# Kernel optimization log

Measured on AMD Instinct MI355X. Metric: run time of the kernel, lower is better.

The kernel has to match this reference:

```python
import jax, jax.numpy as jnp
import numpy as np

LN2 = 0.693147
TARGET_MEAN = 200.0
TARGET_STD = 40.0
BUFFER_SIZE = 1000
TARGET_LOG_MEAN = float(np.log2(TARGET_MEAN))
TARGET_LOG_STD = TARGET_STD / (TARGET_MEAN * LN2)
BLOCK = 33_554_432  # 2**25 pitch frames


def setup_inputs() -> dict:
    key = jax.random.key(0)
    k1, k2 = jax.random.split(key)
    u = jax.random.uniform(k1, (BLOCK,), dtype=jnp.float32)
    unvoiced = jax.random.uniform(k2, (BLOCK,), dtype=jnp.float32) < 0.2
    # realistic F0 range 80-480 Hz, zeros for unvoiced frames
    pitch = jnp.where(unvoiced, 0.0, 80.0 + 400.0 * u)
    return {"pitch_values": pitch}


def reference(pitch_values):
    # State is the freshly-initialized tracker: empty buffer, buffer_idx = 0.
    N = pitch_values.shape[0]
    B = BUFFER_SIZE
    valid = pitch_values > 0
    # log2 of valid pitches (safe for invalid lanes)
    log_p = jnp.log2(jnp.where(valid, pitch_values, 1.0))

    # rank of each valid element among valid elements (scatter order)
    rank = jnp.cumsum(valid.astype(jnp.int32)) - 1          # [N]
    n_valid = jnp.maximum(rank[-1] + 1, 0)
    # dense array of valid log-pitches ordered by rank (unique indices)
    dense_idx = jnp.where(valid, rank, N)                    # N is OOB -> dropped
    dense = jnp.zeros((N,), pitch_values.dtype).at[dense_idx].set(log_p, mode='drop')

    # circular buffer: slot j holds the LAST (max-rank) value written there
    slot = jnp.where(valid, rank % B, B)                     # B is OOB -> dropped
    winner = jnp.full((B,), -1, jnp.int32).at[slot].max(rank, mode='drop')
    filled = winner >= 0
    buf = jnp.where(filled, dense[jnp.clip(winner, 0, N - 1)], 0.0)

    count = jnp.minimum(n_valid, B)
    cnt_f = jnp.maximum(count, 1).astype(pitch_values.dtype)
    mean = jnp.sum(buf) / cnt_f
    mean = jnp.where(count > 0, mean, 0.0)                   # init mean = 0.0
    var = jnp.sum(jnp.where(filled, (buf - mean) ** 2, 0.0)) / jnp.maximum(count - 1, 1).astype(pitch_values.dtype)
    std = jnp.where(count > 1, jnp.sqrt(var), 1.0)           # unbiased std (torch default)
    std = jnp.maximum(std, 1e-7)

    normalized = (log_p - mean) / std
    scaled = normalized * TARGET_LOG_STD + TARGET_LOG_MEAN
    return jnp.where(valid, jnp.exp2(scaled), 0.0)
```

## Files before the change

### kernel.cpp

```cpp
#include <hip/hip_runtime.h>
#include <math.h>

#define BUF_SIZE 1000
#define TARGET_LOG_MEAN 7.6438561897747395f
#define TARGET_LOG_STD  (40.0f / (200.0f * 0.693147f))

__global__ __launch_bounds__(256) void fused_kernel(
    const float* __restrict__ pitch, float* __restrict__ out, long long n) {
    const int tid  = threadIdx.x;
    const int lane = tid & 63;
    const int wid  = tid >> 6;

    __shared__ int    s_wtot[4];
    __shared__ double s_red[8];
    __shared__ float  s_sb[2];

    double sum = 0.0, sumsq = 0.0;
    long long count_so_far = 0;

    const unsigned long long above =
        (lane == 63) ? 0ULL : (~0ULL << (lane + 1));

    const long long nchunks = (n + 1023) >> 10;
    for (long long c = nchunks - 1; c >= 0; --c) {
        const long long base = (c << 10) + (long long)tid * 4;
        float v[4];
        int valid[4];
#pragma unroll
        for (int j = 0; j < 4; ++j) {
            const long long idx = base + j;
            const float p = (idx < n) ? pitch[idx] : 0.0f;
            v[j] = p;
            valid[j] = (p > 0.0f) ? 1 : 0;
        }

        int suff_wave = 0;
        int wtot = 0;
#pragma unroll
        for (int j = 0; j < 4; ++j) {
            const unsigned long long m = __ballot(valid[j]);
            suff_wave += __popcll(m & above);
            wtot      += __popcll(m);
        }
        if (lane == 0) s_wtot[wid] = wtot;
        __syncthreads();
        int suff_after = suff_wave;
        int total = 0;
#pragma unroll
        for (int w = 0; w < 4; ++w) {
            const int t = s_wtot[w];
            total += t;
            if (w > wid) suff_after += t;
        }

        int r = 0;
#pragma unroll
        for (int j = 3; j >= 0; --j) {
            if (valid[j]) {
                const long long rev = count_so_far + suff_after + r;
                if (rev < BUF_SIZE) {
                    const double lp = (double)__log2f(v[j]);
                    sum   += lp;
                    sumsq += lp * lp;
                }
                r++;
            }
        }
        count_so_far += total;
        __syncthreads();
        if (count_so_far >= BUF_SIZE) break;
    }

#pragma unroll
    for (int off = 32; off > 0; off >>= 1) {
        sum   += __shfl_down(sum,   off, 64);
        sumsq += __shfl_down(sumsq, off, 64);
    }
    if (lane == 0) { s_red[wid] = sum; s_red[4 + wid] = sumsq; }
    __syncthreads();
    if (tid == 0) {
        const double tsum   = s_red[0] + s_red[1] + s_red[2] + s_red[3];
        const double tsumsq = s_red[4] + s_red[5] + s_red[6] + s_red[7];
        const long long count =
            (count_so_far < BUF_SIZE) ? count_so_far : BUF_SIZE;
        float mean, stdv;
        if (count == 0) {
            mean = 0.0f;
            stdv = 1.0f;
        } else {
            mean = (float)(tsum / (double)count);
            if (count > 1) {
                double var = (tsumsq - tsum * tsum / (double)count) /
                             (double)(count - 1);
                if (var < 0.0) var = 0.0;
                stdv = (float)sqrt(var);
            } else {
                stdv = 1.0f;
            }
        }
        if (stdv < 1e-7f) stdv = 1e-7f;
        const float scale = TARGET_LOG_STD / stdv;
        s_sb[0] = scale;
        s_sb[1] = TARGET_LOG_MEAN - mean * scale;
    }
    __syncthreads();
    const float scale = s_sb[0];
    const float bias  = s_sb[1];

    const float4* __restrict__ in4  = (const float4*)pitch;
    float4* __restrict__       out4 = (float4*)out;
    const long long n4     = n >> 2;
    const long long gid    = (long long)blockIdx.x * blockDim.x + tid;
    const long long stride = (long long)gridDim.x * blockDim.x;

    for (long long k = gid; k < n4; k += stride) {
        const float4 p = in4[k];
        float4 o;
        o.x = (p.x > 0.0f) ? exp2f(fmaf(__log2f(p.x), scale, bias)) : 0.0f;
        o.y = (p.y > 0.0f) ? exp2f(fmaf(__log2f(p.y), scale, bias)) : 0.0f;
        o.z = (p.z > 0.0f) ? exp2f(fmaf(__log2f(p.z), scale, bias)) : 0.0f;
        o.w = (p.w > 0.0f) ? exp2f(fmaf(__log2f(p.w), scale, bias)) : 0.0f;
        out4[k] = o;
    }

    const long long tail_start = n4 << 2;
    for (long long k = tail_start + gid; k < n; k += stride) {
        const float p = pitch[k];
        out[k] = (p > 0.0f) ? exp2f(fmaf(__log2f(p), scale, bias)) : 0.0f;
    }
}

extern "C" void kernel_launch(void* const* d_in, const int* in_sizes, int n_in,
                              void* d_out, int out_size, void* d_ws, size_t ws_size,
                              hipStream_t stream) {
    const float* pitch = (const float*)d_in[0];
    float* out = (float*)d_out;
    const long long n = (long long)in_sizes[0];

    int blocks = 2048;
    const long long n4 = n / 4;
    if ((long long)blocks * 256 > n4 + 255) {
        blocks = (int)((n4 + 255) / 256);
        if (blocks < 1) blocks = 1;
    }
    fused_kernel<<<blocks, 256, 0, stream>>>(pitch, out, n);
}
```

Baseline: 233.8 us.

## Prefetch first tile before stats scan and software-pipeline the elementwise pass

Each block now issues loads for its first 4 float4 vectors before the backward suffix scan that computes the buffer statistics, so that memory latency overlaps the scan. The main loop is restructured so each thread handles 4 float4 per iteration while prefetching the next iteration's data into registers (double buffering). The backward scan is widened to 8 elements per thread with vector loads, and launch bounds are tightened to 6 waves per SIMD. This raises register pressure in exchange for more memory-level parallelism.

```diff
diff --git a/kernel.cpp b/kernel.cpp
--- a/kernel.cpp
+++ b/kernel.cpp
@@ -5,7 +5,7 @@
 #define TARGET_LOG_MEAN 7.6438561897747395f
 #define TARGET_LOG_STD  (40.0f / (200.0f * 0.693147f))
 
-__global__ __launch_bounds__(256) void fused_kernel(
+__global__ __launch_bounds__(256, 6) void fused_kernel(
     const float* __restrict__ pitch, float* __restrict__ out, long long n) {
     const int tid  = threadIdx.x;
     const int lane = tid & 63;
@@ -15,29 +15,48 @@
     __shared__ double s_red[8];
     __shared__ float  s_sb[2];
 
+    const float4* __restrict__ in4  = (const float4*)pitch;
+    float4* __restrict__       out4 = (float4*)out;
+    const long long n4      = n >> 2;
+    const long long CHUNK4  = 1024;
+    const long long gstride = (long long)gridDim.x * CHUNK4;
+    const long long kbase   = (long long)blockIdx.x * CHUNK4 + tid;
+
+    float4 a0 = {0,0,0,0}, a1 = {0,0,0,0}, a2 = {0,0,0,0}, a3 = {0,0,0,0};
+    if (kbase < n4)       a0 = in4[kbase];
+    if (kbase + 256 < n4) a1 = in4[kbase + 256];
+    if (kbase + 512 < n4) a2 = in4[kbase + 512];
+    if (kbase + 768 < n4) a3 = in4[kbase + 768];
+
     double sum = 0.0, sumsq = 0.0;
     long long count_so_far = 0;
 
     const unsigned long long above =
         (lane == 63) ? 0ULL : (~0ULL << (lane + 1));
 
-    const long long nchunks = (n + 1023) >> 10;
+    const long long nchunks = (n + 2047) >> 11;
     for (long long c = nchunks - 1; c >= 0; --c) {
-        const long long base = (c << 10) + (long long)tid * 4;
-        float v[4];
-        int valid[4];
+        const long long base = (c << 11) + (long long)tid * 8;
+        float v[8];
+        if (base + 8 <= n) {
+            const float4 x = in4[(base >> 2)];
+            const float4 y = in4[(base >> 2) + 1];
+            v[0] = x.x; v[1] = x.y; v[2] = x.z; v[3] = x.w;
+            v[4] = y.x; v[5] = y.y; v[6] = y.z; v[7] = y.w;
+        } else {
 #pragma unroll
-        for (int j = 0; j < 4; ++j) {
-            const long long idx = base + j;
-            const float p = (idx < n) ? pitch[idx] : 0.0f;
-            v[j] = p;
-            valid[j] = (p > 0.0f) ? 1 : 0;
+            for (int j = 0; j < 8; ++j) {
+                const long long idx = base + j;
+                v[j] = (idx < n) ? pitch[idx] : 0.0f;
+            }
         }
 
+        int valid[8];
         int suff_wave = 0;
         int wtot = 0;
 #pragma unroll
-        for (int j = 0; j < 4; ++j) {
+        for (int j = 0; j < 8; ++j) {
+            valid[j] = (v[j] > 0.0f) ? 1 : 0;
             const unsigned long long m = __ballot(valid[j]);
             suff_wave += __popcll(m & above);
             wtot      += __popcll(m);
@@ -55,7 +74,7 @@
 
         int r = 0;
 #pragma unroll
-        for (int j = 3; j >= 0; --j) {
+        for (int j = 7; j >= 0; --j) {
             if (valid[j]) {
                 const long long rev = count_so_far + suff_after + r;
                 if (rev < BUF_SIZE) {
@@ -107,26 +126,48 @@
     const float scale = s_sb[0];
     const float bias  = s_sb[1];
 
-    const float4* __restrict__ in4  = (const float4*)pitch;
-    float4* __restrict__       out4 = (float4*)out;
-    const long long n4     = n >> 2;
-    const long long gid    = (long long)blockIdx.x * blockDim.x + tid;
-    const long long stride = (long long)gridDim.x * blockDim.x;
+    long long k = kbase;
+    while (k < n4) {
+        const long long kn = k + gstride;
+        float4 b0 = {0,0,0,0}, b1 = {0,0,0,0}, b2 = {0,0,0,0}, b3 = {0,0,0,0};
+        if (kn < n4)       b0 = in4[kn];
+        if (kn + 256 < n4) b1 = in4[kn + 256];
+        if (kn + 512 < n4) b2 = in4[kn + 512];
+        if (kn + 768 < n4) b3 = in4[kn + 768];
 
-    for (long long k = gid; k < n4; k += stride) {
-        const float4 p = in4[k];
-        float4 o;
-        o.x = (p.x > 0.0f) ? exp2f(fmaf(__log2f(p.x), scale, bias)) : 0.0f;
-        o.y = (p.y > 0.0f) ? exp2f(fmaf(__log2f(p.y), scale, bias)) : 0.0f;
-        o.z = (p.z > 0.0f) ? exp2f(fmaf(__log2f(p.z), scale, bias)) : 0.0f;
-        o.w = (p.w > 0.0f) ? exp2f(fmaf(__log2f(p.w), scale, bias)) : 0.0f;
-        out4[k] = o;
+        float4 o0, o1, o2, o3;
+        o0.x = (a0.x > 0.0f) ? exp2f(fmaf(__log2f(a0.x), scale, bias)) : 0.0f;
+        o0.y = (a0.y > 0.0f) ? exp2f(fmaf(__log2f(a0.y), scale, bias)) : 0.0f;
+        o0.z = (a0.z > 0.0f) ? exp2f(fmaf(__log2f(a0.z), scale, bias)) : 0.0f;
+        o0.w = (a0.w > 0.0f) ? exp2f(fmaf(__log2f(a0.w), scale, bias)) : 0.0f;
+        o1.x = (a1.x > 0.0f) ? exp2f(fmaf(__log2f(a1.x), scale, bias)) : 0.0f;
+        o1.y = (a1.y > 0.0f) ? exp2f(fmaf(__log2f(a1.y), scale, bias)) : 0.0f;
+        o1.z = (a1.z > 0.0f) ? exp2f(fmaf(__log2f(a1.z), scale, bias)) : 0.0f;
+        o1.w = (a1.w > 0.0f) ? exp2f(fmaf(__log2f(a1.w), scale, bias)) : 0.0f;
+        o2.x = (a2.x > 0.0f) ? exp2f(fmaf(__log2f(a2.x), scale, bias)) : 0.0f;
+        o2.y = (a2.y > 0.0f) ? exp2f(fmaf(__log2f(a2.y), scale, bias)) : 0.0f;
+        o2.z = (a2.z > 0.0f) ? exp2f(fmaf(__log2f(a2.z), scale, bias)) : 0.0f;
+        o2.w = (a2.w > 0.0f) ? exp2f(fmaf(__log2f(a2.w), scale, bias)) : 0.0f;
+        o3.x = (a3.x > 0.0f) ? exp2f(fmaf(__log2f(a3.x), scale, bias)) : 0.0f;
+        o3.y = (a3.y > 0.0f) ? exp2f(fmaf(__log2f(a3.y), scale, bias)) : 0.0f;
+        o3.z = (a3.z > 0.0f) ? exp2f(fmaf(__log2f(a3.z), scale, bias)) : 0.0f;
+        o3.w = (a3.w > 0.0f) ? exp2f(fmaf(__log2f(a3.w), scale, bias)) : 0.0f;
+
+        out4[k] = o0;
+        if (k + 256 < n4) out4[k + 256] = o1;
+        if (k + 512 < n4) out4[k + 512] = o2;
+        if (k + 768 < n4) out4[k + 768] = o3;
+
+        a0 = b0; a1 = b1; a2 = b2; a3 = b3;
+        k = kn;
     }
 
     const long long tail_start = n4 << 2;
-    for (long long k = tail_start + gid; k < n; k += stride) {
-        const float p = pitch[k];
-        out[k] = (p > 0.0f) ? exp2f(fmaf(__log2f(p), scale, bias)) : 0.0f;
+    const long long gid     = (long long)blockIdx.x * 256 + tid;
+    const long long tstride = (long long)gridDim.x * 256;
+    for (long long t = tail_start + gid; t < n; t += tstride) {
+        const float p = pitch[t];
+        out[t] = (p > 0.0f) ? exp2f(fmaf(__log2f(p), scale, bias)) : 0.0f;
     }
 }
 
@@ -137,11 +178,9 @@
     float* out = (float*)d_out;
     const long long n = (long long)in_sizes[0];
 
-    int blocks = 2048;
     const long long n4 = n / 4;
-    if ((long long)blocks * 256 > n4 + 255) {
-        blocks = (int)((n4 + 255) / 256);
-        if (blocks < 1) blocks = 1;
-    }
+    long long want = (n4 + 1023) / 1024;
+    int blocks = (int)((want < 2048) ? want : 2048);
+    if (blocks < 1) blocks = 1;
     fused_kernel<<<blocks, 256, 0, stream>>>(pitch, out, n);
 }
```

Result: faster. 229.1 us (-2.0%).

## Split stats pass into single-block kernel and launch separate wide apply kernel

Applied to the files above, without the earlier changes.

The fused kernel previously had every block redundantly scan the tail of the input to compute the buffer statistics before applying the transform. This splits it into a single-block stats kernel that writes scale and bias to workspace, followed by a separate elementwise kernel with up to 32768 blocks. The stats scan now processes 8 elements per thread with float4 loads. This removes the redundant per-block scan and its contention, at the cost of an extra kernel launch and a serial dependency between the two kernels.

```diff
diff --git a/kernel.cpp b/kernel.cpp
--- a/kernel.cpp
+++ b/kernel.cpp
@@ -5,15 +5,17 @@
 #define TARGET_LOG_MEAN 7.6438561897747395f
 #define TARGET_LOG_STD  (40.0f / (200.0f * 0.693147f))
 
-__global__ __launch_bounds__(256) void fused_kernel(
-    const float* __restrict__ pitch, float* __restrict__ out, long long n) {
+
+__global__ __launch_bounds__(256) void stats_kernel(
+    const float* __restrict__ pitch, long long n, float* __restrict__ stats) {
     const int tid  = threadIdx.x;
     const int lane = tid & 63;
     const int wid  = tid >> 6;
 
     __shared__ int    s_wtot[4];
     __shared__ double s_red[8];
-    __shared__ float  s_sb[2];
+
+    const float4* __restrict__ in4 = (const float4*)pitch;
 
     double sum = 0.0, sumsq = 0.0;
     long long count_so_far = 0;
@@ -21,23 +23,29 @@
     const unsigned long long above =
         (lane == 63) ? 0ULL : (~0ULL << (lane + 1));
 
-    const long long nchunks = (n + 1023) >> 10;
+    const long long nchunks = (n + 2047) >> 11;
     for (long long c = nchunks - 1; c >= 0; --c) {
-        const long long base = (c << 10) + (long long)tid * 4;
-        float v[4];
-        int valid[4];
+        const long long base = (c << 11) + (long long)tid * 8;
+        float v[8];
+        if (base + 8 <= n) {
+            const float4 x = in4[(base >> 2)];
+            const float4 y = in4[(base >> 2) + 1];
+            v[0] = x.x; v[1] = x.y; v[2] = x.z; v[3] = x.w;
+            v[4] = y.x; v[5] = y.y; v[6] = y.z; v[7] = y.w;
+        } else {
 #pragma unroll
-        for (int j = 0; j < 4; ++j) {
-            const long long idx = base + j;
-            const float p = (idx < n) ? pitch[idx] : 0.0f;
-            v[j] = p;
-            valid[j] = (p > 0.0f) ? 1 : 0;
+            for (int j = 0; j < 8; ++j) {
+                const long long idx = base + j;
+                v[j] = (idx < n) ? pitch[idx] : 0.0f;
+            }
         }
 
+        int valid[8];
         int suff_wave = 0;
         int wtot = 0;
 #pragma unroll
-        for (int j = 0; j < 4; ++j) {
+        for (int j = 0; j < 8; ++j) {
+            valid[j] = (v[j] > 0.0f) ? 1 : 0;
             const unsigned long long m = __ballot(valid[j]);
             suff_wave += __popcll(m & above);
             wtot      += __popcll(m);
@@ -55,7 +63,7 @@
 
         int r = 0;
 #pragma unroll
-        for (int j = 3; j >= 0; --j) {
+        for (int j = 7; j >= 0; --j) {
             if (valid[j]) {
                 const long long rev = count_so_far + suff_after + r;
                 if (rev < BUF_SIZE) {
@@ -100,17 +108,19 @@
         }
         if (stdv < 1e-7f) stdv = 1e-7f;
         const float scale = TARGET_LOG_STD / stdv;
-        s_sb[0] = scale;
-        s_sb[1] = TARGET_LOG_MEAN - mean * scale;
+        stats[0] = scale;
+        stats[1] = TARGET_LOG_MEAN - mean * scale;
     }
-    __syncthreads();
-    const float scale = s_sb[0];
-    const float bias  = s_sb[1];
+}
 
-    const float4* __restrict__ in4  = (const float4*)pitch;
-    float4* __restrict__       out4 = (float4*)out;
-    const long long n4     = n >> 2;
-    const long long gid    = (long long)blockIdx.x * blockDim.x + tid;
+__global__ void apply_kernel(const float4* __restrict__ in4,
+                             float4* __restrict__ out4, long long n4,
+                             const float* __restrict__ pitch,
+                             float* __restrict__ out, long long n,
+                             const float* __restrict__ stats) {
+    const float scale = stats[0];
+    const float bias = stats[1];
+    const long long gid = (long long)blockIdx.x * blockDim.x + threadIdx.x;
     const long long stride = (long long)gridDim.x * blockDim.x;
 
     for (long long k = gid; k < n4; k += stride) {
@@ -123,7 +133,7 @@
         out4[k] = o;
     }
 
-    const long long tail_start = n4 << 2;
+    const long long tail_start = n4 * 4;
     for (long long k = tail_start + gid; k < n; k += stride) {
         const float p = pitch[k];
         out[k] = (p > 0.0f) ? exp2f(fmaf(__log2f(p), scale, bias)) : 0.0f;
@@ -136,12 +146,14 @@
     const float* pitch = (const float*)d_in[0];
     float* out = (float*)d_out;
     const long long n = (long long)in_sizes[0];
+    float* stats = (float*)d_ws;
 
-    int blocks = 2048;
+    stats_kernel<<<1, 256, 0, stream>>>(pitch, n, stats);
+
     const long long n4 = n / 4;
-    if ((long long)blocks * 256 > n4 + 255) {
-        blocks = (int)((n4 + 255) / 256);
-        if (blocks < 1) blocks = 1;
-    }
-    fused_kernel<<<blocks, 256, 0, stream>>>(pitch, out, n);
+    int blocks = (int)((n4 + 255) / 256);
+    if (blocks > 32768) blocks = 32768;
+    if (blocks < 1) blocks = 1;
+    apply_kernel<<<blocks, 256, 0, stream>>>((const float4*)pitch, (float4*)out,
+                                             n4, pitch, out, n, stats);
 }
```

Measured after the change: 225.1 us. 3.7% less time.
